# Optimization experiments

Hardware: AMD Instinct MI355X
Metric: run time of the kernel (lower is better)

## Reference

```python
import jax, jax.numpy as jnp
import numpy as np

N_NODES = 100000
N_EDGES = 1600000
D_IN, D_HID, D_OUT = 256, 512, 48
K_STEPS = 10
ALPHA = 0.1


def setup_inputs() -> dict:
    key = jax.random.key(0)
    k_x, k_e, k_w1, k_w2 = jax.random.split(key, 4)
    x = jax.random.normal(k_x, (N_NODES, D_IN), dtype=jnp.float32)
    edge_index = jax.random.randint(k_e, (2, N_EDGES), 0, N_NODES, dtype=jnp.int64)
    # MLP params (Kaiming-ish scaling)
    W1 = jax.random.normal(k_w1, (D_IN, D_HID), dtype=jnp.float32) * (1.0 / np.sqrt(D_IN))
    b1 = jnp.zeros((D_HID,), dtype=jnp.float32)
    W2 = jax.random.normal(k_w2, (D_HID, D_OUT), dtype=jnp.float32) * (1.0 / np.sqrt(D_HID))
    b2 = jnp.zeros((D_OUT,), dtype=jnp.float32)
    return {"x": x, "edge_index": edge_index, "W1": W1, "b1": b1, "W2": W2, "b2": b2}


def reference(x, edge_index, W1, b1, W2, b2):
    N = x.shape[0]
    # --- MLP encoder ---
    h = jax.nn.relu(x @ W1 + b1) @ W2 + b2  # [N, D_OUT]

    # --- APPNP propagation (PyG defaults: add self-loops, symmetric gcn_norm) ---
    loop = jnp.arange(N, dtype=edge_index.dtype)
    src = jnp.concatenate([edge_index[0], loop])  # [E+N]
    dst = jnp.concatenate([edge_index[1], loop])
    ones = jnp.ones(src.shape[0], dtype=h.dtype)
    deg = jax.ops.segment_sum(ones, dst, num_segments=N)  # in-degree incl. self-loop
    dinv = jnp.where(deg > 0, jax.lax.rsqrt(deg), 0.0)
    norm = dinv[src] * dinv[dst]  # [E+N]

    out = h
    for _ in range(K_STEPS):
        msg = out[src] * norm[:, None]                      # gather + scale
        agg = jax.ops.segment_sum(msg, dst, num_segments=N)  # scatter-add
        out = (1.0 - ALPHA) * agg + ALPHA * h                # teleport mix
    return out
```

## Files before the change

### kernel.cpp

```cpp
#include <hip/hip_runtime.h>
#include <hip/hip_fp16.h>

constexpr int D_IN = 256, D_HID = 512, D_OUT = 48;
constexpr int HPAD = 64;
constexpr int K_STEPS = 10;

typedef __attribute__((ext_vector_type(8))) __bf16 bf16x8;
typedef __attribute__((ext_vector_type(4))) float f32x4;

__device__ __forceinline__ unsigned short f2bf(float f) {
  unsigned u = __builtin_bit_cast(unsigned, f);
  u += 0x7fffu + ((u >> 16) & 1u);
  return (unsigned short)(u >> 16);
}

__device__ __forceinline__ void gl2lds16(const unsigned short* g, unsigned short* l) {
  __builtin_amdgcn_global_load_lds(
      (const __attribute__((address_space(1))) unsigned int*)g,
      (__attribute__((address_space(3))) unsigned int*)l, 16, 0, 0);
}


__global__ void zero2_kernel(int* __restrict__ a, int* __restrict__ b, int N) {
  int i = blockIdx.x * 256 + threadIdx.x;
  if (i < N) { a[i] = 0; b[i] = 0; }
}

__global__ __launch_bounds__(256) void count_kernel(const int* __restrict__ dst,
                                                    int* __restrict__ cnt, int E) {
  int team = blockIdx.x & 7;
  int bt = blockIdx.x >> 3;
  int step = (gridDim.x >> 3) * 256;
  for (int e = bt * 256 + threadIdx.x; e < E; e += step) {
    int d = dst[e];
    if (((d >> 12) & 7) == team) atomicAdd(&cnt[d], 1);
  }
}

__global__ void dinv_kernel(const int* __restrict__ cnt, float* __restrict__ dinv, int N) {
  int n = blockIdx.x * 256 + threadIdx.x;
  if (n < N) dinv[n] = rsqrtf((float)(cnt[n] + 1));
}

__global__ void scan1_kernel(const int* __restrict__ cnt, int* __restrict__ row_ptr,
                             int* __restrict__ bsum, int N) {
  __shared__ int sd[256];
  int tid = threadIdx.x, b = blockIdx.x;
  int i0 = b * 1024 + tid * 4;
  int v[4];
#pragma unroll
  for (int m = 0; m < 4; ++m) v[m] = (i0 + m < N) ? ((cnt[i0 + m] + 3) & ~3) : 0;
  int s = v[0] + v[1] + v[2] + v[3];
  sd[tid] = s;
  __syncthreads();
  for (int off = 1; off < 256; off <<= 1) {
    int t = (tid >= off) ? sd[tid - off] : 0;
    __syncthreads();
    sd[tid] += t;
    __syncthreads();
  }
  int run = sd[tid] - s;
#pragma unroll
  for (int m = 0; m < 4; ++m) {
    if (i0 + m < N) row_ptr[i0 + m] = run;
    run += v[m];
  }
  if (tid == 255) bsum[b] = sd[255];
}

__global__ void scan2_kernel(const int* __restrict__ bsum, int* __restrict__ bofs,
                             int* __restrict__ row_ptr, int NB, int N) {
  __shared__ int sd[128];
  int tid = threadIdx.x;
  int v = (tid < NB) ? bsum[tid] : 0;
  sd[tid] = v;
  __syncthreads();
  for (int off = 1; off < 128; off <<= 1) {
    int t = (tid >= off) ? sd[tid - off] : 0;
    __syncthreads();
    sd[tid] += t;
    __syncthreads();
  }
  if (tid < NB) bofs[tid] = sd[tid] - v;
  if (tid == 127) row_ptr[N] = sd[127];
}

__global__ void scan3_kernel(int* __restrict__ row_ptr, const int* __restrict__ bofs, int N) {
  int b = blockIdx.x;
  if (b == 0) return;
  int add = bofs[b];
  int i0 = b * 1024 + threadIdx.x * 4;
#pragma unroll
  for (int m = 0; m < 4; ++m)
    if (i0 + m < N) row_ptr[i0 + m] += add;
}

__global__ __launch_bounds__(256) void fill_kernel(
    const int* __restrict__ src, const int* __restrict__ dst,
    const int* __restrict__ row_ptr, int* __restrict__ cnt2,
    const float* __restrict__ dinv, int2* __restrict__ edges, int E) {
  int team = blockIdx.x & 7;
  int bt = blockIdx.x >> 3;
  int step = (gridDim.x >> 3) * 256;
  for (int e = bt * 256 + threadIdx.x; e < E; e += step) {
    int d = dst[e];
    if (((d >> 12) & 7) != team) continue;
    int s = src[e];
    int p = row_ptr[d] + atomicAdd(&cnt2[d], 1);
    edges[p] = make_int2(s, __float_as_int(dinv[s]));
  }
}

__global__ void pad_kernel(const int* __restrict__ cnt, const int* __restrict__ row_ptr,
                           int2* __restrict__ edges, int N) {
  int n = blockIdx.x * 256 + threadIdx.x;
  if (n >= N) return;
  int a = row_ptr[n] + cnt[n];
  int b = row_ptr[n + 1];
  for (int p = a; p < b; ++p) edges[p] = make_int2(n, 0);
}


__global__ void convert_w1(const float* __restrict__ W1, unsigned short* __restrict__ W1F) {
  int i = blockIdx.x * 256 + threadIdx.x;
  if (i >= D_HID * D_IN) return;
  int c = i >> 8, k = i & 255;
  int ct = c >> 6, tn = (c >> 4) & 3, l15 = c & 15;
  int kb = k >> 5, q = (k >> 3) & 3, j = k & 7;
  int lane = (q << 4) | l15;
  int dst = (((ct * 4 + tn) * 8 + kb) << 9) + lane * 8 + j;
  W1F[dst] = f2bf(W1[k * D_HID + c]);
}

__global__ void convert_w2(const float* __restrict__ W2, unsigned short* __restrict__ W2F) {
  int i = blockIdx.x * 256 + threadIdx.x;
  if (i >= D_OUT * D_HID) return;
  int n = i >> 9, k = i & 511;
  int ct = k >> 6, kk = (k >> 5) & 1, q = (k >> 3) & 3, j = k & 7;
  int tn = n >> 4, l15 = n & 15;
  int lane = (q << 4) | l15;
  int dst = (((ct * 2 + kk) * 3 + tn) << 9) + lane * 8 + j;
  W2F[dst] = f2bf(W2[k * D_OUT + n]);
}


__global__ __launch_bounds__(512, 4) void encoder_kernel(
    const float* __restrict__ x, const float* __restrict__ b1,
    const float* __restrict__ b2,
    const unsigned short* __restrict__ W1F,
    const unsigned short* __restrict__ W2F,
    __half* __restrict__ h2, int N) {
  __shared__ unsigned short sW1[16384];
  __shared__ unsigned short sHid[8][16][72];
  __shared__ float sB1[512];
  __shared__ float sB2[64];

  int tid = threadIdx.x;
  int w = tid >> 6, lane = tid & 63;
  int q = lane >> 4, l15 = lane & 15;
  int row0 = blockIdx.x * 128 + w * 16;

  {
    const unsigned short* gsrc = W1F + (w << 9) + lane * 8;
    unsigned short* ldst = &sW1[w << 9];
#pragma unroll
    for (int i = 0; i < 4; ++i)
      gl2lds16(gsrc + (i << 12), ldst + (i << 12));
  }
  sB1[tid] = b1[tid];
  if (tid < 48) sB2[tid] = b2[tid];

  int grow = row0 + l15;
  bool rok = grow < N;
  const float* xr = x + (size_t)grow * D_IN;
  float4 xv[16];
#pragma unroll
  for (int jb = 0; jb < 8; ++jb) {
    xv[2 * jb]     = rok ? *(const float4*)(xr + jb * 32 + q * 8)
                         : make_float4(0.f, 0.f, 0.f, 0.f);
    xv[2 * jb + 1] = rok ? *(const float4*)(xr + jb * 32 + q * 8 + 4)
                         : make_float4(0.f, 0.f, 0.f, 0.f);
  }
  uint4 axu[8];
#pragma unroll
  for (int jb = 0; jb < 8; ++jb) {
    union { uint4 u; unsigned short s[8]; } uu;
    float4 v0 = xv[2 * jb], v1 = xv[2 * jb + 1];
    uu.s[0] = f2bf(v0.x); uu.s[1] = f2bf(v0.y); uu.s[2] = f2bf(v0.z); uu.s[3] = f2bf(v0.w);
    uu.s[4] = f2bf(v1.x); uu.s[5] = f2bf(v1.y); uu.s[6] = f2bf(v1.z); uu.s[7] = f2bf(v1.w);
    axu[jb] = uu.u;
  }

  f32x4 hacc[3];
#pragma unroll
  for (int t = 0; t < 3; ++t)
#pragma unroll
    for (int r = 0; r < 4; ++r) hacc[t][r] = 0.f;

  __syncthreads();

  for (int ct = 0; ct < 8; ++ct) {
    int c0 = ct * 64;
    f32x4 acc[4];
#pragma unroll
    for (int t = 0; t < 4; ++t)
#pragma unroll
      for (int r = 0; r < 4; ++r) acc[t][r] = 0.f;

    const unsigned short* sb = &sW1[lane * 8];
#pragma unroll
    for (int kb = 0; kb < 8; ++kb) {
      bf16x8 a = __builtin_bit_cast(bf16x8, axu[kb]);
      bf16x8 bq0 = *(const bf16x8*)(sb + (kb << 9));
      bf16x8 bq1 = *(const bf16x8*)(sb + (kb << 9) + 4096);
      bf16x8 bq2 = *(const bf16x8*)(sb + (kb << 9) + 8192);
      bf16x8 bq3 = *(const bf16x8*)(sb + (kb << 9) + 12288);
      acc[0] = __builtin_amdgcn_mfma_f32_16x16x32_bf16(a, bq0, acc[0], 0, 0, 0);
      acc[1] = __builtin_amdgcn_mfma_f32_16x16x32_bf16(a, bq1, acc[1], 0, 0, 0);
      acc[2] = __builtin_amdgcn_mfma_f32_16x16x32_bf16(a, bq2, acc[2], 0, 0, 0);
      acc[3] = __builtin_amdgcn_mfma_f32_16x16x32_bf16(a, bq3, acc[3], 0, 0, 0);
    }
#pragma unroll
    for (int tn = 0; tn < 4; ++tn) {
      int c = tn * 16 + l15;
      float bias = sB1[c0 + c];
#pragma unroll
      for (int rg = 0; rg < 4; ++rg) {
        float v = acc[tn][rg] + bias;
        v = v > 0.f ? v : 0.f;
        sHid[w][q * 4 + rg][c] = f2bf(v);
      }
    }
#pragma unroll
    for (int kk = 0; kk < 2; ++kk) {
      bf16x8 a0 = *(const bf16x8*)&sHid[w][l15][kk * 32 + q * 8];
      const unsigned short* w2b = W2F + (((ct * 2 + kk) * 3) << 9) + lane * 8;
#pragma unroll
      for (int tn = 0; tn < 3; ++tn) {
        bf16x8 b = *(const bf16x8*)(w2b + (tn << 9));
        hacc[tn] = __builtin_amdgcn_mfma_f32_16x16x32_bf16(a0, b, hacc[tn], 0, 0, 0);
      }
    }
    __syncthreads();
    if (ct < 7) {
      const unsigned short* gsrc = W1F + ((size_t)(ct + 1) << 14) + (w << 9) + lane * 8;
      unsigned short* ldst = &sW1[w << 9];
#pragma unroll
      for (int i = 0; i < 4; ++i)
        gl2lds16(gsrc + (i << 12), ldst + (i << 12));
      __syncthreads();
    }
  }
#pragma unroll
  for (int tn = 0; tn < 3; ++tn) {
    int c = tn * 16 + l15;
    float bias = sB2[c];
#pragma unroll
    for (int rg = 0; rg < 4; ++rg) {
      int gr = row0 + q * 4 + rg;
      if (gr < N) h2[(size_t)gr * HPAD + c] = __float2half(hacc[tn][rg] + bias);
    }
  }
#pragma unroll
  for (int rg = 0; rg < 4; ++rg) {
    int gr = row0 + q * 4 + rg;
    if (gr < N) h2[(size_t)gr * HPAD + 48 + l15] = __float2half(0.f);
  }
}


__global__ __launch_bounds__(256) void prop_kernel(
    const __half* __restrict__ cur, const __half* __restrict__ h2,
    const float* __restrict__ dinv, const int* __restrict__ row_ptr,
    const int2* __restrict__ edges, __half* __restrict__ nxt,
    float* __restrict__ outf, int N, int last) {
  int wid = (blockIdx.x * 256 + threadIdx.x) >> 6;
  int lane = threadIdx.x & 63;
  int half = lane >> 5;
  int slot = (lane >> 3) & 3;
  int s = lane & 7;
  int node = wid * 2 + half;
  bool nok = node < N;
  int p0 = 0, p1 = 0;
  if (nok) { int2 pp = *(const int2*)(row_ptr + node); p0 = pp.x; p1 = pp.y; }
  int d = p1 - p0;
  int dmax = max(d, __shfl_xor(d, 32));
  int nb = dmax >> 2;

  float acc[8];
#pragma unroll
  for (int i = 0; i < 8; ++i) acc[i] = 0.f;

  int p = p0 + slot;
  int2 e0 = make_int2(0, 0), e1 = make_int2(0, 0);
  if (nb > 0) e0 = edges[p];
  if (nb > 1) e1 = edges[p + 4];
  int b = 0;
  for (; b + 2 <= nb; b += 2) {
    int2 n0 = make_int2(0, 0), n1 = make_int2(0, 0);
    if (b + 2 < nb) n0 = edges[p + 8];
    if (b + 3 < nb) n1 = edges[p + 12];
    float w0 = (p < p1) ? __int_as_float(e0.y) : 0.f;
    float w1 = (p + 4 < p1) ? __int_as_float(e1.y) : 0.f;
    union { float4 f; __half2 h[4]; } u0, u1;
    u0.f = *(const float4*)(cur + ((size_t)e0.x << 6) + s * 8);
    u1.f = *(const float4*)(cur + ((size_t)e1.x << 6) + s * 8);
#pragma unroll
    for (int i = 0; i < 4; ++i) {
      float2 f0 = __half22float2(u0.h[i]);
      float2 f1 = __half22float2(u1.h[i]);
      acc[2 * i]     += w0 * f0.x + w1 * f1.x;
      acc[2 * i + 1] += w0 * f0.y + w1 * f1.y;
    }
    e0 = n0; e1 = n1; p += 8;
  }
  if (b < nb) {
    float w0 = (p < p1) ? __int_as_float(e0.y) : 0.f;
    union { float4 f; __half2 h[4]; } u0;
    u0.f = *(const float4*)(cur + ((size_t)e0.x << 6) + s * 8);
#pragma unroll
    for (int i = 0; i < 4; ++i) {
      float2 f0 = __half22float2(u0.h[i]);
      acc[2 * i]     += w0 * f0.x;
      acc[2 * i + 1] += w0 * f0.y;
    }
  }
#pragma unroll
  for (int i = 0; i < 8; ++i) {
    acc[i] += __int_as_float(__builtin_amdgcn_ds_swizzle(__float_as_int(acc[i]), 0x201F));
    acc[i] += __int_as_float(__builtin_amdgcn_ds_swizzle(__float_as_int(acc[i]), 0x401F));
  }
  if ((lane & 24) != 0 || !nok) return;
  float di = dinv[node];
  size_t base = ((size_t)node << 6) + s * 8;
  union { float4 f; __half2 h[4]; } us, uh;
  us.f = *(const float4*)(cur + base);
  uh.f = *(const float4*)(h2 + base);
  float dii = di * di;
  float outv[8];
#pragma unroll
  for (int i = 0; i < 4; ++i) {
    float2 sf = __half22float2(us.h[i]);
    float2 hf = __half22float2(uh.h[i]);
    outv[2 * i]     = 0.9f * (di * acc[2 * i]     + dii * sf.x) + 0.1f * hf.x;
    outv[2 * i + 1] = 0.9f * (di * acc[2 * i + 1] + dii * sf.y) + 0.1f * hf.y;
  }
  if (last) {
    if (s < 6) {
      float* op = outf + (size_t)node * D_OUT + s * 8;
      *(float4*)op       = make_float4(outv[0], outv[1], outv[2], outv[3]);
      *(float4*)(op + 4) = make_float4(outv[4], outv[5], outv[6], outv[7]);
    }
  } else {
    union { uint4 u4; __half2 h[4]; } o;
#pragma unroll
    for (int i = 0; i < 4; ++i) o.h[i] = __floats2half2_rn(outv[2 * i], outv[2 * i + 1]);
    *(uint4*)(nxt + base) = o.u4;
  }
}


extern "C" void kernel_launch(void* const* d_in, const int* in_sizes, int n_in,
                              void* d_out, int out_size, void* d_ws, size_t ws_size,
                              hipStream_t stream) {
  (void)n_in; (void)out_size; (void)ws_size;
  const float* x  = (const float*)d_in[0];
  const int*   ei = (const int*)d_in[1];
  const float* W1 = (const float*)d_in[2];
  const float* b1 = (const float*)d_in[3];
  const float* W2 = (const float*)d_in[4];
  const float* b2 = (const float*)d_in[5];
  const int N = in_sizes[0] / D_IN;
  const int E = in_sizes[1] / 2;
  const int* e_src = ei;
  const int* e_dst = ei + E;

  char* ws = (char*)d_ws;
  size_t off = 0;
  auto take = [&](size_t bytes) -> char* {
    char* p = ws + off;
    off += (bytes + 511) & ~(size_t)511;
    return p;
  };
  int* cnt      = (int*)take((size_t)N * 4);
  int* cnt2     = (int*)take((size_t)N * 4);
  float* dinv   = (float*)take((size_t)N * 4);
  int* row_ptr  = (int*)take((size_t)(N + 1) * 4);
  int* bsum     = (int*)take(1024);
  int* bofs     = (int*)take(1024);
  int2* edges   = (int2*)take(((size_t)E + 4 * (size_t)N) * 8);
  unsigned short* W1F = (unsigned short*)take((size_t)D_IN * D_HID * 2);
  unsigned short* W2F = (unsigned short*)take((size_t)D_HID * D_OUT * 2);
  __half* h2    = (__half*)take((size_t)N * HPAD * 2);
  __half* bufA  = (__half*)take((size_t)N * HPAD * 2);
  __half* bufB  = (__half*)d_out;
  float* outp   = (float*)d_out;

  int nb256 = (N + 255) / 256;
  int eb256 = (E + 255) / 256;
  int NB    = (N + 1023) / 1024;

  zero2_kernel<<<nb256, 256, 0, stream>>>(cnt, cnt2, N);
  count_kernel<<<2048, 256, 0, stream>>>(e_dst, cnt, E);
  dinv_kernel<<<nb256, 256, 0, stream>>>(cnt, dinv, N);
  scan1_kernel<<<NB, 256, 0, stream>>>(cnt, row_ptr, bsum, N);
  scan2_kernel<<<1, 128, 0, stream>>>(bsum, bofs, row_ptr, NB, N);
  scan3_kernel<<<NB, 256, 0, stream>>>(row_ptr, bofs, N);
  fill_kernel<<<2048, 256, 0, stream>>>(e_src, e_dst, row_ptr, cnt2, dinv, edges, E);
  pad_kernel<<<nb256, 256, 0, stream>>>(cnt, row_ptr, edges, N);

  convert_w1<<<(D_IN * D_HID + 255) / 256, 256, 0, stream>>>(W1, W1F);
  convert_w2<<<(D_HID * D_OUT + 255) / 256, 256, 0, stream>>>(W2, W2F);
  encoder_kernel<<<(N + 127) / 128, 512, 0, stream>>>(x, b1, b2, W1F, W2F, h2, N);

  int waves = (N + 1) / 2;
  int pblocks = (waves + 3) / 4;
  const __half* src = h2;
  __half* dst = bufA;
  for (int it = 1; it <= K_STEPS; ++it) {
    int last = (it == K_STEPS);
    prop_kernel<<<pblocks, 256, 0, stream>>>(src, h2, dinv, row_ptr, edges,
                                             dst, outp, N, last);
    src = dst;
    dst = (dst == bufA) ? bufB : bufA;
  }
}
```

Measured before the change: 714.8 us.

## Prescale features by dinv, store bare column indices, use atomic-rank CSR build

The propagation now keeps features prescaled by dinv, so each edge becomes an unweighted gather-add. The edge list shrinks from int2 (index, weight) to int, and the self-loop is folded into the CSR row. Padding slots point to a zero row at index N, which replaces the per-edge weight masking. The CSR build drops the 8-team atomic scheme and instead records each edge's rank from the count atomics, so the fill pass needs no atomics. In exchange the code adds a rank array, an extra zero-row kernel, an extra qb write in the encoder, and an extra rounding of the prescaled fp16 values.

```diff
diff --git a/kernel.cpp b/kernel.cpp
--- a/kernel.cpp
+++ b/kernel.cpp
@@ -21,20 +21,19 @@
 }
 
 
-__global__ void zero2_kernel(int* __restrict__ a, int* __restrict__ b, int N) {
+__global__ void zero1_kernel(int* __restrict__ a, int N) {
   int i = blockIdx.x * 256 + threadIdx.x;
-  if (i < N) { a[i] = 0; b[i] = 0; }
+  if (i < N) a[i] = 0;
 }
 
 __global__ __launch_bounds__(256) void count_kernel(const int* __restrict__ dst,
-                                                    int* __restrict__ cnt, int E) {
-  int team = blockIdx.x & 7;
-  int bt = blockIdx.x >> 3;
-  int step = (gridDim.x >> 3) * 256;
-  for (int e = bt * 256 + threadIdx.x; e < E; e += step) {
-    int d = dst[e];
-    if (((d >> 12) & 7) == team) atomicAdd(&cnt[d], 1);
-  }
+                                                    int* __restrict__ cnt,
+                                                    int* __restrict__ rank, int E) {
+  int e = blockIdx.x * 256 + threadIdx.x;
+  if (e >= E) return;
+  int d = __builtin_nontemporal_load(dst + e);
+  int r = atomicAdd(&cnt[d], 1);
+  __builtin_nontemporal_store(r, rank + e);
 }
 
 __global__ void dinv_kernel(const int* __restrict__ cnt, float* __restrict__ dinv, int N) {
@@ -49,7 +48,7 @@
   int i0 = b * 1024 + tid * 4;
   int v[4];
 #pragma unroll
-  for (int m = 0; m < 4; ++m) v[m] = (i0 + m < N) ? ((cnt[i0 + m] + 3) & ~3) : 0;
+  for (int m = 0; m < 4; ++m) v[m] = (i0 + m < N) ? ((cnt[i0 + m] + 4) & ~3) : 0;
   int s = v[0] + v[1] + v[2] + v[3];
   sd[tid] = s;
   __syncthreads();
@@ -97,27 +96,30 @@
 
 __global__ __launch_bounds__(256) void fill_kernel(
     const int* __restrict__ src, const int* __restrict__ dst,
-    const int* __restrict__ row_ptr, int* __restrict__ cnt2,
-    const float* __restrict__ dinv, int2* __restrict__ edges, int E) {
-  int team = blockIdx.x & 7;
-  int bt = blockIdx.x >> 3;
-  int step = (gridDim.x >> 3) * 256;
-  for (int e = bt * 256 + threadIdx.x; e < E; e += step) {
-    int d = dst[e];
-    if (((d >> 12) & 7) != team) continue;
-    int s = src[e];
-    int p = row_ptr[d] + atomicAdd(&cnt2[d], 1);
-    edges[p] = make_int2(s, __float_as_int(dinv[s]));
-  }
+    const int* __restrict__ row_ptr, const int* __restrict__ rank,
+    int* __restrict__ edges, int E) {
+  int e = blockIdx.x * 256 + threadIdx.x;
+  if (e >= E) return;
+  int d = __builtin_nontemporal_load(dst + e);
+  int s = __builtin_nontemporal_load(src + e);
+  int r = __builtin_nontemporal_load(rank + e);
+  edges[row_ptr[d] + r] = s;
 }
 
 __global__ void pad_kernel(const int* __restrict__ cnt, const int* __restrict__ row_ptr,
-                           int2* __restrict__ edges, int N) {
+                           int* __restrict__ edges, int N) {
   int n = blockIdx.x * 256 + threadIdx.x;
   if (n >= N) return;
   int a = row_ptr[n] + cnt[n];
   int b = row_ptr[n + 1];
-  for (int p = a; p < b; ++p) edges[p] = make_int2(n, 0);
+  edges[a] = n;
+  for (int p = a + 1; p < b; ++p) edges[p] = N;
+}
+
+__global__ void zrow_kernel(__half* __restrict__ a, __half* __restrict__ b, int N) {
+  int t = threadIdx.x;
+  a[(size_t)N * HPAD + t] = __float2half(0.f);
+  b[(size_t)N * HPAD + t] = __float2half(0.f);
 }
 
 
@@ -146,10 +148,10 @@
 
 __global__ __launch_bounds__(512, 4) void encoder_kernel(
     const float* __restrict__ x, const float* __restrict__ b1,
-    const float* __restrict__ b2,
+    const float* __restrict__ b2, const float* __restrict__ dinvp,
     const unsigned short* __restrict__ W1F,
     const unsigned short* __restrict__ W2F,
-    __half* __restrict__ h2, int N) {
+    __half* __restrict__ h2, __half* __restrict__ qb, int N) {
   __shared__ unsigned short sW1[16384];
   __shared__ unsigned short sHid[8][16][72];
   __shared__ float sB1[512];
@@ -251,6 +253,12 @@
       __syncthreads();
     }
   }
+  float dv[4];
+#pragma unroll
+  for (int rg = 0; rg < 4; ++rg) {
+    int gr = row0 + q * 4 + rg;
+    dv[rg] = (gr < N) ? dinvp[gr] : 0.f;
+  }
 #pragma unroll
   for (int tn = 0; tn < 3; ++tn) {
     int c = tn * 16 + l15;
@@ -258,13 +266,20 @@
 #pragma unroll
     for (int rg = 0; rg < 4; ++rg) {
       int gr = row0 + q * 4 + rg;
-      if (gr < N) h2[(size_t)gr * HPAD + c] = __float2half(hacc[tn][rg] + bias);
+      if (gr < N) {
+        float val = hacc[tn][rg] + bias;
+        h2[(size_t)gr * HPAD + c] = __float2half(val);
+        qb[(size_t)gr * HPAD + c] = __float2half(dv[rg] * val);
+      }
     }
   }
 #pragma unroll
   for (int rg = 0; rg < 4; ++rg) {
     int gr = row0 + q * 4 + rg;
-    if (gr < N) h2[(size_t)gr * HPAD + 48 + l15] = __float2half(0.f);
+    if (gr < N) {
+      h2[(size_t)gr * HPAD + 48 + l15] = __float2half(0.f);
+      qb[(size_t)gr * HPAD + 48 + l15] = __float2half(0.f);
+    }
   }
 }
 
@@ -272,7 +287,7 @@
 __global__ __launch_bounds__(256) void prop_kernel(
     const __half* __restrict__ cur, const __half* __restrict__ h2,
     const float* __restrict__ dinv, const int* __restrict__ row_ptr,
-    const int2* __restrict__ edges, __half* __restrict__ nxt,
+    const int* __restrict__ edges, __half* __restrict__ nxt,
     float* __restrict__ outf, int N, int last) {
   int wid = (blockIdx.x * 256 + threadIdx.x) >> 6;
   int lane = threadIdx.x & 63;
@@ -292,37 +307,37 @@
   for (int i = 0; i < 8; ++i) acc[i] = 0.f;
 
   int p = p0 + slot;
-  int2 e0 = make_int2(0, 0), e1 = make_int2(0, 0);
+  int e0 = N, e1 = N;
   if (nb > 0) e0 = edges[p];
   if (nb > 1) e1 = edges[p + 4];
   int b = 0;
   for (; b + 2 <= nb; b += 2) {
-    int2 n0 = make_int2(0, 0), n1 = make_int2(0, 0);
+    int n0 = N, n1 = N;
     if (b + 2 < nb) n0 = edges[p + 8];
     if (b + 3 < nb) n1 = edges[p + 12];
-    float w0 = (p < p1) ? __int_as_float(e0.y) : 0.f;
-    float w1 = (p + 4 < p1) ? __int_as_float(e1.y) : 0.f;
+    int i0 = (p < p1) ? e0 : N;
+    int i1 = (p + 4 < p1) ? e1 : N;
     union { float4 f; __half2 h[4]; } u0, u1;
-    u0.f = *(const float4*)(cur + ((size_t)e0.x << 6) + s * 8);
-    u1.f = *(const float4*)(cur + ((size_t)e1.x << 6) + s * 8);
+    u0.f = *(const float4*)(cur + ((size_t)i0 << 6) + s * 8);
+    u1.f = *(const float4*)(cur + ((size_t)i1 << 6) + s * 8);
 #pragma unroll
     for (int i = 0; i < 4; ++i) {
       float2 f0 = __half22float2(u0.h[i]);
       float2 f1 = __half22float2(u1.h[i]);
-      acc[2 * i]     += w0 * f0.x + w1 * f1.x;
-      acc[2 * i + 1] += w0 * f0.y + w1 * f1.y;
+      acc[2 * i]     += f0.x + f1.x;
+      acc[2 * i + 1] += f0.y + f1.y;
     }
     e0 = n0; e1 = n1; p += 8;
   }
   if (b < nb) {
-    float w0 = (p < p1) ? __int_as_float(e0.y) : 0.f;
+    int i0 = (p < p1) ? e0 : N;
     union { float4 f; __half2 h[4]; } u0;
-    u0.f = *(const float4*)(cur + ((size_t)e0.x << 6) + s * 8);
+    u0.f = *(const float4*)(cur + ((size_t)i0 << 6) + s * 8);
 #pragma unroll
     for (int i = 0; i < 4; ++i) {
       float2 f0 = __half22float2(u0.h[i]);
-      acc[2 * i]     += w0 * f0.x;
-      acc[2 * i + 1] += w0 * f0.y;
+      acc[2 * i]     += f0.x;
+      acc[2 * i + 1] += f0.y;
     }
   }
 #pragma unroll
@@ -333,17 +348,14 @@
   if ((lane & 24) != 0 || !nok) return;
   float di = dinv[node];
   size_t base = ((size_t)node << 6) + s * 8;
-  union { float4 f; __half2 h[4]; } us, uh;
-  us.f = *(const float4*)(cur + base);
+  union { float4 f; __half2 h[4]; } uh;
   uh.f = *(const float4*)(h2 + base);
-  float dii = di * di;
   float outv[8];
 #pragma unroll
   for (int i = 0; i < 4; ++i) {
-    float2 sf = __half22float2(us.h[i]);
     float2 hf = __half22float2(uh.h[i]);
-    outv[2 * i]     = 0.9f * (di * acc[2 * i]     + dii * sf.x) + 0.1f * hf.x;
-    outv[2 * i + 1] = 0.9f * (di * acc[2 * i + 1] + dii * sf.y) + 0.1f * hf.y;
+    outv[2 * i]     = 0.9f * di * acc[2 * i]     + 0.1f * hf.x;
+    outv[2 * i + 1] = 0.9f * di * acc[2 * i + 1] + 0.1f * hf.y;
   }
   if (last) {
     if (s < 6) {
@@ -354,7 +366,8 @@
   } else {
     union { uint4 u4; __half2 h[4]; } o;
 #pragma unroll
-    for (int i = 0; i < 4; ++i) o.h[i] = __floats2half2_rn(outv[2 * i], outv[2 * i + 1]);
+    for (int i = 0; i < 4; ++i)
+      o.h[i] = __floats2half2_rn(di * outv[2 * i], di * outv[2 * i + 1]);
     *(uint4*)(nxt + base) = o.u4;
   }
 }
@@ -383,16 +396,16 @@
     return p;
   };
   int* cnt      = (int*)take((size_t)N * 4);
-  int* cnt2     = (int*)take((size_t)N * 4);
   float* dinv   = (float*)take((size_t)N * 4);
   int* row_ptr  = (int*)take((size_t)(N + 1) * 4);
   int* bsum     = (int*)take(1024);
   int* bofs     = (int*)take(1024);
-  int2* edges   = (int2*)take(((size_t)E + 4 * (size_t)N) * 8);
+  int* rank     = (int*)take((size_t)E * 4);
+  int* edges    = (int*)take(((size_t)E + 4 * (size_t)N + 1024) * 4);
   unsigned short* W1F = (unsigned short*)take((size_t)D_IN * D_HID * 2);
   unsigned short* W2F = (unsigned short*)take((size_t)D_HID * D_OUT * 2);
   __half* h2    = (__half*)take((size_t)N * HPAD * 2);
-  __half* bufA  = (__half*)take((size_t)N * HPAD * 2);
+  __half* bufA  = (__half*)take((size_t)(N + 1) * HPAD * 2);
   __half* bufB  = (__half*)d_out;
   float* outp   = (float*)d_out;
 
@@ -400,22 +413,24 @@
   int eb256 = (E + 255) / 256;
   int NB    = (N + 1023) / 1024;
 
-  zero2_kernel<<<nb256, 256, 0, stream>>>(cnt, cnt2, N);
-  count_kernel<<<2048, 256, 0, stream>>>(e_dst, cnt, E);
+  zero1_kernel<<<nb256, 256, 0, stream>>>(cnt, N);
+  count_kernel<<<eb256, 256, 0, stream>>>(e_dst, cnt, rank, E);
   dinv_kernel<<<nb256, 256, 0, stream>>>(cnt, dinv, N);
   scan1_kernel<<<NB, 256, 0, stream>>>(cnt, row_ptr, bsum, N);
   scan2_kernel<<<1, 128, 0, stream>>>(bsum, bofs, row_ptr, NB, N);
   scan3_kernel<<<NB, 256, 0, stream>>>(row_ptr, bofs, N);
-  fill_kernel<<<2048, 256, 0, stream>>>(e_src, e_dst, row_ptr, cnt2, dinv, edges, E);
+  fill_kernel<<<eb256, 256, 0, stream>>>(e_src, e_dst, row_ptr, rank, edges, E);
   pad_kernel<<<nb256, 256, 0, stream>>>(cnt, row_ptr, edges, N);
+  zrow_kernel<<<1, 64, 0, stream>>>(bufA, bufB, N);
 
   convert_w1<<<(D_IN * D_HID + 255) / 256, 256, 0, stream>>>(W1, W1F);
   convert_w2<<<(D_HID * D_OUT + 255) / 256, 256, 0, stream>>>(W2, W2F);
-  encoder_kernel<<<(N + 127) / 128, 512, 0, stream>>>(x, b1, b2, W1F, W2F, h2, N);
+  encoder_kernel<<<(N + 127) / 128, 512, 0, stream>>>(x, b1, b2, dinv, W1F, W2F,
+                                                      h2, bufB, N);
 
   int waves = (N + 1) / 2;
   int pblocks = (waves + 3) / 4;
-  const __half* src = h2;
+  const __half* src = bufB;
   __half* dst = bufA;
   for (int it = 1; it <= K_STEPS; ++it) {
     int last = (it == K_STEPS);
```

Result: faster. 668.9 us (-6.4%).
